# Performance work log

Measured on AMD Instinct MI355X. Metric: run time of the kernel, lower is better.

## Reference

```python
import jax, jax.numpy as jnp
import numpy as np

N = 50000
E = 800000
F_IN = 128
H = 8        # heads
C = 32       # hidden_channels per head
HC = H * C   # 256
NEG_SLOPE = 0.2


def setup_inputs() -> dict:
    key = jax.random.key(0)
    ks = jax.random.split(key, 16)
    s = 0.1
    return {
        'x': jax.random.normal(ks[0], (N, F_IN), jnp.float32),
        'edge_index': jax.random.randint(ks[1], (2, E), 0, N, jnp.int64),
        'edge_weights': jax.random.uniform(ks[2], (E,), jnp.float32),
        'W1': jax.random.normal(ks[3], (F_IN, HC), jnp.float32) * s,
        'att_src1': jax.random.normal(ks[4], (H, C), jnp.float32) * s,
        'att_dst1': jax.random.normal(ks[5], (H, C), jnp.float32) * s,
        'b1': jnp.zeros((HC,), jnp.float32),
        'W2': jax.random.normal(ks[6], (HC, HC), jnp.float32) * s,
        'att_src2': jax.random.normal(ks[7], (H, C), jnp.float32) * s,
        'att_dst2': jax.random.normal(ks[8], (H, C), jnp.float32) * s,
        'b2': jnp.zeros((HC,), jnp.float32),
        'We': jax.random.normal(ks[9], (HC, 1), jnp.float32) * s,
        'be': jnp.zeros((1,), jnp.float32),
        'Wn': jax.random.normal(ks[10], (HC, 1), jnp.float32) * s,
        'bn': jnp.zeros((1,), jnp.float32),
    }


def gat_conv(x, src, dst, W, att_src, att_dst, bias):
    """PyG GATConv (concat=True, eval mode, self-loops already in src/dst)."""
    n = x.shape[0]
    h = (x @ W).reshape(n, H, C)                      # [N,H,C]
    a_s = jnp.sum(h * att_src, axis=-1)               # [N,H]
    a_d = jnp.sum(h * att_dst, axis=-1)               # [N,H]
    e = jax.nn.leaky_relu(a_s[src] + a_d[dst], NEG_SLOPE)  # [E',H]
    m = jax.ops.segment_max(e, dst, num_segments=n)   # segment softmax over dst
    ex = jnp.exp(e - m[dst])
    denom = jax.ops.segment_sum(ex, dst, num_segments=n)
    alpha = ex / (denom[dst] + 1e-16)                 # [E',H]
    out = jax.ops.segment_sum(alpha[..., None] * h[src], dst, num_segments=n)
    return out.reshape(n, HC) + bias


def reference(x, edge_index, edge_weights, W1, att_src1, att_dst1, b1,
              W2, att_src2, att_dst2, b2, We, be, Wn, bn):
    src0, dst0 = edge_index[0], edge_index[1]
    loops = jnp.arange(N, dtype=src0.dtype)
    src = jnp.concatenate([src0, loops])
    dst = jnp.concatenate([dst0, loops])
    # edge_weights is passed to GATConv as edge_attr but unused (edge_dim=None)
    h = jax.nn.relu(gat_conv(x, src, dst, W1, att_src1, att_dst1, b1))
    h = jax.nn.relu(gat_conv(h, src, dst, W2, att_src2, att_dst2, b2))
    edge_pred = (h[src0] * h[dst0]) @ We + be          # [E,1]
    node_pred = h @ Wn + bn                            # [N,1]
    return (edge_pred, node_pred)
```

## Files before the change

kernel.cpp:

```cpp
#include <hip/hip_runtime.h>
#include <hip/hip_bf16.h>

#define NN 50000
#define NE 800000
#define FIN 128
#define HC 256
#define NEG_SLOPE 0.2f

#define GEMM_BLOCKS 782
#define NSB 3321
#define NB_ZERO 196
#define NB_X 6250
#define NB_W1 128
#define NB_W2 256

typedef short bf16x8 __attribute__((ext_vector_type(8)));
typedef float f32x4 __attribute__((ext_vector_type(4)));

__device__ __forceinline__ unsigned short f2bf(float f) {
  unsigned u = __float_as_uint(f);
  u += 0x7fff + ((u >> 16) & 1);
  return (unsigned short)(u >> 16);
}
__device__ __forceinline__ float bf2f(unsigned short s) {
  return __uint_as_float((unsigned)s << 16);
}
__device__ __forceinline__ float bflo(unsigned u) { return __uint_as_float(u << 16); }
__device__ __forceinline__ float bfhi(unsigned u) { return __uint_as_float(u & 0xffff0000u); }

__global__ __launch_bounds__(256) void prep_kernel(
    const float* __restrict__ X, unsigned short* __restrict__ Xh,
    const float* __restrict__ W1, unsigned short* __restrict__ W1th,
    unsigned short* __restrict__ W1tl, const float* __restrict__ W2,
    unsigned short* __restrict__ W2th, unsigned short* __restrict__ W2tl,
    int* __restrict__ counts, int* __restrict__ tmp) {
  int b = blockIdx.x, t = threadIdx.x;
  if (b < NB_ZERO) {
    int i = b * 256 + t;
    if (i < NN) { counts[i] = 0; tmp[i] = 0; }
  } else if (b < NB_ZERO + NB_X) {
    int i = (b - NB_ZERO) * 256 + t;
    float4 v = ((const float4*)X)[i];
    ushort4 h;
    h.x = f2bf(v.x); h.y = f2bf(v.y); h.z = f2bf(v.z); h.w = f2bf(v.w);
    ((ushort4*)Xh)[i] = h;
  } else if (b < NB_ZERO + NB_X + NB_W1) {
    int j = (b - NB_ZERO - NB_X) * 256 + t;
    int n = j >> 7, k = j & 127;
    float v = W1[k * HC + n];
    unsigned short h = f2bf(v);
    W1th[j] = h;
    W1tl[j] = f2bf(v - bf2f(h));
  } else {
    int j = (b - NB_ZERO - NB_X - NB_W1) * 256 + t;
    int n = j >> 8, k = j & 255;
    float v = W2[k * HC + n];
    unsigned short h = f2bf(v);
    W2th[j] = h;
    W2tl[j] = f2bf(v - bf2f(h));
  }
}

__global__ __launch_bounds__(256) void gemm_coef(
    const unsigned short* __restrict__ A, const unsigned short* __restrict__ Bth,
    const unsigned short* __restrict__ Btl, const float* __restrict__ att_s,
    const float* __restrict__ att_d, unsigned short* __restrict__ Cb,
    float* __restrict__ a_s, float* __restrict__ a_d, int M, int K,
    const int* __restrict__ ei, const int* __restrict__ rowptr,
    int* __restrict__ tmpc, int2* __restrict__ ce) {
  __shared__ unsigned short smem[128 * 136];

  int bid = blockIdx.x, t = threadIdx.x;
  if (bid >= GEMM_BLOCKS) {
    int e = (bid - GEMM_BLOCKS) * 256 + t;
    if (e < NE + NN) {
      int s, d, id;
      if (e < NE) { s = ei[e]; d = ei[NE + e]; id = e; }
      else { s = d = e - NE; id = -1; }
      int pos = rowptr[d] + atomicAdd(&tmpc[d], 1);
      ce[pos] = make_int2(s, id);
    }
    return;
  }

  int w = t >> 6, lane = t & 63;
  int quad = lane >> 4, lrow = lane & 15;
  int m0 = (bid >> 1) * 128, n0 = (bid & 1) * 128;
  int wm = (w >> 1) * 64, wn = (w & 1) * 64;

  const unsigned short* arow[4];
#pragma unroll
  for (int mi = 0; mi < 4; ++mi) {
    int gm = m0 + wm + mi * 16 + lrow;
    if (gm >= M) gm = M - 1;
    arow[mi] = A + (size_t)gm * K + quad * 8;
  }

  f32x4 acc[4][4] = {};

  for (int k0 = 0; k0 < K; k0 += 32) {
#pragma unroll
    for (int i = 0; i < 2; ++i) {
      int idx = t + i * 256;
      int row = idx >> 2, q = idx & 3;
      size_t gb = (size_t)(n0 + row) * K + k0 + q * 8;
      *(uint4*)(smem + row * 40 + q * 8) = *(const uint4*)(Bth + gb);
      *(uint4*)(smem + 5120 + row * 40 + q * 8) = *(const uint4*)(Btl + gb);
    }
    __syncthreads();

    bf16x8 fa[4];
#pragma unroll
    for (int mi = 0; mi < 4; ++mi) fa[mi] = *(const bf16x8*)(arow[mi] + k0);
#pragma unroll
    for (int ni = 0; ni < 4; ++ni) {
      bf16x8 fbh = *(const bf16x8*)(smem + (wn + ni * 16 + lrow) * 40 + quad * 8);
      bf16x8 fbl = *(const bf16x8*)(smem + 5120 + (wn + ni * 16 + lrow) * 40 + quad * 8);
#pragma unroll
      for (int mi = 0; mi < 4; ++mi) {
        acc[mi][ni] = __builtin_amdgcn_mfma_f32_16x16x32_bf16(fa[mi], fbh, acc[mi][ni], 0, 0, 0);
        acc[mi][ni] = __builtin_amdgcn_mfma_f32_16x16x32_bf16(fa[mi], fbl, acc[mi][ni], 0, 0, 0);
      }
    }
    __syncthreads();
  }

#pragma unroll
  for (int mi = 0; mi < 4; ++mi) {
#pragma unroll
    for (int r = 0; r < 4; ++r) {
      int row = wm + mi * 16 + quad * 4 + r;
#pragma unroll
      for (int ni = 0; ni < 4; ++ni) {
        int col = wn + ni * 16 + lrow;
        smem[row * 136 + col] = f2bf(acc[mi][ni][r]);
      }
    }
  }
  __syncthreads();

  {
    int row = t >> 1, half = t & 1;
    int gm = m0 + row;
    if (gm < M) {
      float ps0 = 0.f, ps1 = 0.f, pd0 = 0.f, pd1 = 0.f;
#pragma unroll
      for (int j = 0; j < 8; ++j) {
        uint4 v = *(const uint4*)(smem + row * 136 + half * 64 + j * 8);
        int gc = n0 + half * 64 + j * 8;
        *(uint4*)(Cb + (size_t)gm * HC + gc) = v;
        float4 s0 = *(const float4*)(att_s + gc);
        float4 s1 = *(const float4*)(att_s + gc + 4);
        float4 d0 = *(const float4*)(att_d + gc);
        float4 d1 = *(const float4*)(att_d + gc + 4);
        float f0 = bflo(v.x), f1 = bfhi(v.x), f2 = bflo(v.y), f3 = bfhi(v.y);
        float f4 = bflo(v.z), f5 = bfhi(v.z), f6 = bflo(v.w), f7 = bfhi(v.w);
        float ss = f0 * s0.x + f1 * s0.y + f2 * s0.z + f3 * s0.w +
                   f4 * s1.x + f5 * s1.y + f6 * s1.z + f7 * s1.w;
        float dd = f0 * d0.x + f1 * d0.y + f2 * d0.z + f3 * d0.w +
                   f4 * d1.x + f5 * d1.y + f6 * d1.z + f7 * d1.w;
        if (j < 4) { ps0 += ss; pd0 += dd; }
        else       { ps1 += ss; pd1 += dd; }
      }
      int hb2 = (n0 >> 5) + half * 2;
      a_s[gm * 8 + hb2] = ps0;
      a_s[gm * 8 + hb2 + 1] = ps1;
      a_d[gm * 8 + hb2] = pd0;
      a_d[gm * 8 + hb2 + 1] = pd1;
    }
  }
}

__global__ void hist_kernel(const int* __restrict__ ei, int* __restrict__ counts) {
  int e = blockIdx.x * 256 + threadIdx.x;
  if (e < NE) atomicAdd(&counts[ei[NE + e]], 1);
}

__global__ void scan1(const int* __restrict__ counts, int* __restrict__ scanbuf,
                      int* __restrict__ bsum) {
  __shared__ int sd[256];
  int t = threadIdx.x;
  int i = blockIdx.x * 256 + t;
  int v = (i < NN) ? counts[i] + 1 : 0;
  sd[t] = v;
  __syncthreads();
#pragma unroll
  for (int off = 1; off < 256; off <<= 1) {
    int x = (t >= off) ? sd[t - off] : 0;
    __syncthreads();
    sd[t] += x;
    __syncthreads();
  }
  if (i < NN) scanbuf[i] = sd[t];
  if (t == 255) bsum[blockIdx.x] = sd[255];
}

__global__ void scan2(const int* __restrict__ bsum, int* __restrict__ boff, int nb) {
  __shared__ int sd[256];
  int t = threadIdx.x;
  int v = (t < nb) ? bsum[t] : 0;
  sd[t] = v;
  __syncthreads();
#pragma unroll
  for (int off = 1; off < 256; off <<= 1) {
    int x = (t >= off) ? sd[t - off] : 0;
    __syncthreads();
    sd[t] += x;
    __syncthreads();
  }
  if (t < nb) boff[t] = sd[t] - v;
}

__global__ void scan3(const int* __restrict__ scanbuf, const int* __restrict__ boff,
                      int* __restrict__ rowptr) {
  int i = blockIdx.x * 256 + threadIdx.x;
  if (i < NN) rowptr[i + 1] = scanbuf[i] + boff[blockIdx.x];
  if (i == 0) rowptr[0] = 0;
}

__global__ __launch_bounds__(256) void agg_kernel(
    const unsigned short* __restrict__ htb, const float* __restrict__ a_s,
    const float* __restrict__ a_d, const int* __restrict__ rowptr,
    const int2* __restrict__ ce, const float* __restrict__ bias,
    unsigned short* __restrict__ outb,
    const float* __restrict__ Wn, const float* __restrict__ bn,
    float* __restrict__ outn) {
  int d = blockIdx.x * 8 + (threadIdx.x >> 5);
  if (d >= NN) return;
  int l = threadIdx.x & 31;
  int hh = l >> 2;
  float adh = a_d[d * 8 + hh];
  int r0 = rowptr[d], r1 = rowptr[d + 1];
  float denom = 0.f;
  float4 acc0 = {0.f, 0.f, 0.f, 0.f};
  float4 acc1 = {0.f, 0.f, 0.f, 0.f};
  for (int r = r0; r < r1; r += 4) {
    int s[4];
    float as_[4];
    uint4 q[4];
    bool ok[4];
#pragma unroll
    for (int j = 0; j < 4; ++j) {
      int rj = r + j;
      ok[j] = rj < r1;
      rj = ok[j] ? rj : r1 - 1;
      s[j] = ce[rj].x;
    }
#pragma unroll
    for (int j = 0; j < 4; ++j) {
      as_[j] = a_s[s[j] * 8 + hh];
      q[j] = ((const uint4*)(htb + (size_t)s[j] * HC))[l];
    }
#pragma unroll
    for (int j = 0; j < 4; ++j) {
      float e = as_[j] + adh;
      e = e > 0.f ? e : NEG_SLOPE * e;
      float w = ok[j] ? __expf(e) : 0.f;
      denom += w;
      acc0.x += w * bflo(q[j].x);
      acc0.y += w * bfhi(q[j].x);
      acc0.z += w * bflo(q[j].y);
      acc0.w += w * bfhi(q[j].y);
      acc1.x += w * bflo(q[j].z);
      acc1.y += w * bfhi(q[j].z);
      acc1.z += w * bflo(q[j].w);
      acc1.w += w * bfhi(q[j].w);
    }
  }
  float dv = 1.f / denom;
  float4 b0 = *(const float4*)(bias + l * 8);
  float4 b1 = *(const float4*)(bias + l * 8 + 4);
  float4 o0, o1;
  o0.x = fmaxf(fmaf(acc0.x, dv, b0.x), 0.f);
  o0.y = fmaxf(fmaf(acc0.y, dv, b0.y), 0.f);
  o0.z = fmaxf(fmaf(acc0.z, dv, b0.z), 0.f);
  o0.w = fmaxf(fmaf(acc0.w, dv, b0.w), 0.f);
  o1.x = fmaxf(fmaf(acc1.x, dv, b1.x), 0.f);
  o1.y = fmaxf(fmaf(acc1.y, dv, b1.y), 0.f);
  o1.z = fmaxf(fmaf(acc1.z, dv, b1.z), 0.f);
  o1.w = fmaxf(fmaf(acc1.w, dv, b1.w), 0.f);
  uint4 pb;
  pb.x = (unsigned)f2bf(o0.x) | ((unsigned)f2bf(o0.y) << 16);
  pb.y = (unsigned)f2bf(o0.z) | ((unsigned)f2bf(o0.w) << 16);
  pb.z = (unsigned)f2bf(o1.x) | ((unsigned)f2bf(o1.y) << 16);
  pb.w = (unsigned)f2bf(o1.z) | ((unsigned)f2bf(o1.w) << 16);
  ((uint4*)(outb + (size_t)d * HC))[l] = pb;
  if (outn) {
    const float4* wnp = (const float4*)(Wn + l * 8);
    float4 w0 = wnp[0], w1 = wnp[1];
    float p = o0.x * w0.x + o0.y * w0.y + o0.z * w0.z + o0.w * w0.w +
              o1.x * w1.x + o1.y * w1.y + o1.z * w1.z + o1.w * w1.w;
#pragma unroll
    for (int off = 1; off <= 16; off <<= 1) p += __shfl_xor(p, off);
    if (l == 0) outn[d] = p + bn[0];
  }
}

__global__ __launch_bounds__(256) void edge_pred_kernel(
    const unsigned short* __restrict__ h2b, const int* __restrict__ rowptr,
    const int2* __restrict__ ce, const float* __restrict__ We,
    const float* __restrict__ be, float* __restrict__ out) {
  int d = blockIdx.x * 4 + (threadIdx.x >> 6);
  if (d >= NN) return;
  int lane = threadIdx.x & 63;
  int g = lane >> 4, l = lane & 15;
  float b = be[0];

  const uint4* rowd = (const uint4*)(h2b + (size_t)d * HC + l * 16);
  uint4 qd0 = rowd[0], qd1 = rowd[1];
  float wd[16];
  {
    const float4* wep = (const float4*)(We + l * 16);
    float4 w0 = wep[0], w1 = wep[1], w2 = wep[2], w3 = wep[3];
    wd[0] = bflo(qd0.x) * w0.x;  wd[1] = bfhi(qd0.x) * w0.y;
    wd[2] = bflo(qd0.y) * w0.z;  wd[3] = bfhi(qd0.y) * w0.w;
    wd[4] = bflo(qd0.z) * w1.x;  wd[5] = bfhi(qd0.z) * w1.y;
    wd[6] = bflo(qd0.w) * w1.z;  wd[7] = bfhi(qd0.w) * w1.w;
    wd[8] = bflo(qd1.x) * w2.x;  wd[9] = bfhi(qd1.x) * w2.y;
    wd[10] = bflo(qd1.y) * w2.z; wd[11] = bfhi(qd1.y) * w2.w;
    wd[12] = bflo(qd1.z) * w3.x; wd[13] = bfhi(qd1.z) * w3.y;
    wd[14] = bflo(qd1.w) * w3.z; wd[15] = bfhi(qd1.w) * w3.w;
  }

  int r0 = rowptr[d], r1 = rowptr[d + 1];
  for (int r = r0; r < r1; r += 8) {
    int rr0 = r + g, rr1 = r + 4 + g;
    int s0 = 0, id0 = -1, s1 = 0, id1 = -1;
    if (rr0 < r1) { int2 p = ce[rr0]; s0 = p.x; id0 = p.y; }
    if (rr1 < r1) { int2 p = ce[rr1]; s1 = p.x; id1 = p.y; }
    const uint4* ra = (const uint4*)(h2b + (size_t)s0 * HC + l * 16);
    const uint4* rb = (const uint4*)(h2b + (size_t)s1 * HC + l * 16);
    uint4 a0 = ra[0], a1 = ra[1];
    uint4 c0 = rb[0], c1 = rb[1];
    float p0 = bflo(a0.x) * wd[0] + bfhi(a0.x) * wd[1] + bflo(a0.y) * wd[2] +
               bfhi(a0.y) * wd[3] + bflo(a0.z) * wd[4] + bfhi(a0.z) * wd[5] +
               bflo(a0.w) * wd[6] + bfhi(a0.w) * wd[7] + bflo(a1.x) * wd[8] +
               bfhi(a1.x) * wd[9] + bflo(a1.y) * wd[10] + bfhi(a1.y) * wd[11] +
               bflo(a1.z) * wd[12] + bfhi(a1.z) * wd[13] + bflo(a1.w) * wd[14] +
               bfhi(a1.w) * wd[15];
    float p1 = bflo(c0.x) * wd[0] + bfhi(c0.x) * wd[1] + bflo(c0.y) * wd[2] +
               bfhi(c0.y) * wd[3] + bflo(c0.z) * wd[4] + bfhi(c0.z) * wd[5] +
               bflo(c0.w) * wd[6] + bfhi(c0.w) * wd[7] + bflo(c1.x) * wd[8] +
               bfhi(c1.x) * wd[9] + bflo(c1.y) * wd[10] + bfhi(c1.y) * wd[11] +
               bflo(c1.z) * wd[12] + bfhi(c1.z) * wd[13] + bflo(c1.w) * wd[14] +
               bfhi(c1.w) * wd[15];
#pragma unroll
    for (int off = 1; off <= 8; off <<= 1) {
      p0 += __shfl_xor(p0, off);
      p1 += __shfl_xor(p1, off);
    }
    if (l == 0) {
      if (id0 >= 0) out[id0] = p0 + b;
      if (id1 >= 0) out[id1] = p1 + b;
    }
  }
}

extern "C" void kernel_launch(void* const* d_in, const int* in_sizes, int n_in,
                              void* d_out, int out_size, void* d_ws, size_t ws_size,
                              hipStream_t stream) {
  const float* x  = (const float*)d_in[0];
  const int* ei   = (const int*)d_in[1];
  const float* W1 = (const float*)d_in[3];
  const float* as1 = (const float*)d_in[4];
  const float* ad1 = (const float*)d_in[5];
  const float* b1 = (const float*)d_in[6];
  const float* W2 = (const float*)d_in[7];
  const float* as2 = (const float*)d_in[8];
  const float* ad2 = (const float*)d_in[9];
  const float* b2 = (const float*)d_in[10];
  const float* We = (const float*)d_in[11];
  const float* be = (const float*)d_in[12];
  const float* Wn = (const float*)d_in[13];
  const float* bn = (const float*)d_in[14];
  float* out = (float*)d_out;

  char* wsp = (char*)d_ws;
  auto alloc = [&](size_t bytes) {
    char* p = wsp;
    wsp += (bytes + 255) & ~(size_t)255;
    return p;
  };
  unsigned short* hbA = (unsigned short*)alloc((size_t)NN * HC * 2);
  unsigned short* h1b = (unsigned short*)alloc((size_t)NN * HC * 2);
  unsigned short* hbB = (unsigned short*)alloc((size_t)NN * HC * 2);
  float* a_s = (float*)alloc((size_t)NN * 8 * 4);
  float* a_d = (float*)alloc((size_t)NN * 8 * 4);
  int* rowptr = (int*)alloc((size_t)(NN + 1) * 4);
  int2* ce = (int2*)alloc((size_t)(NE + NN + 8) * 8);
  int* counts = (int*)alloc((size_t)NN * 4);
  int* tmp = (int*)alloc((size_t)NN * 4);
  int* scanbuf = (int*)alloc((size_t)NN * 4);
  int* bsum = (int*)alloc(256 * 4);
  int* boff = (int*)alloc(256 * 4);
  unsigned short* W1th = (unsigned short*)alloc((size_t)FIN * HC * 2);
  unsigned short* W1tl = (unsigned short*)alloc((size_t)FIN * HC * 2);
  unsigned short* W2th = (unsigned short*)alloc((size_t)HC * HC * 2);
  unsigned short* W2tl = (unsigned short*)alloc((size_t)HC * HC * 2);

  unsigned short* xh = h1b;

  const int NB = (NN + 255) / 256;

  prep_kernel<<<NB_ZERO + NB_X + NB_W1 + NB_W2, 256, 0, stream>>>(
      x, xh, W1, W1th, W1tl, W2, W2th, W2tl, counts, tmp);
  hist_kernel<<<(NE + 255) / 256, 256, 0, stream>>>(ei, counts);
  scan1<<<NB, 256, 0, stream>>>(counts, scanbuf, bsum);
  scan2<<<1, 256, 0, stream>>>(bsum, boff, NB);
  scan3<<<NB, 256, 0, stream>>>(scanbuf, boff, rowptr);

  gemm_coef<<<GEMM_BLOCKS + NSB, 256, 0, stream>>>(
      xh, W1th, W1tl, as1, ad1, hbA, a_s, a_d, NN, FIN, ei, rowptr, tmp, ce);
  agg_kernel<<<NN / 8, 256, 0, stream>>>(hbA, a_s, a_d, rowptr, ce, b1, h1b,
                                         (const float*)nullptr, (const float*)nullptr,
                                         (float*)nullptr);

  gemm_coef<<<GEMM_BLOCKS, 256, 0, stream>>>(
      h1b, W2th, W2tl, as2, ad2, hbA, a_s, a_d, NN, HC,
      (const int*)nullptr, rowptr, tmp, ce);
  agg_kernel<<<NN / 8, 256, 0, stream>>>(hbA, a_s, a_d, rowptr, ce, b2, hbB,
                                         Wn, bn, out + NE);

  edge_pred_kernel<<<NN / 4, 256, 0, stream>>>(hbB, rowptr, ce, We, be, out);
}
```

Measured before the change: 460.6 us.

## Stage A tile in LDS and compute attention coefficients from accumulators via shuffles

New measurement: 446.3 us. 3.1% less time.

```diff
diff --git a/kernel.cpp b/kernel.cpp
--- a/kernel.cpp
+++ b/kernel.cpp
@@ -68,7 +68,9 @@
     float* __restrict__ a_s, float* __restrict__ a_d, int M, int K,
     const int* __restrict__ ei, const int* __restrict__ rowptr,
     int* __restrict__ tmpc, int2* __restrict__ ce) {
-  __shared__ unsigned short smem[128 * 136];
+  __shared__ unsigned short sA[128 * 40];
+  __shared__ unsigned short sBh[128 * 40];
+  __shared__ unsigned short sBl[128 * 40];
 
   int bid = blockIdx.x, t = threadIdx.x;
   if (bid >= GEMM_BLOCKS) {
@@ -88,14 +90,6 @@
   int m0 = (bid >> 1) * 128, n0 = (bid & 1) * 128;
   int wm = (w >> 1) * 64, wn = (w & 1) * 64;
 
-  const unsigned short* arow[4];
-#pragma unroll
-  for (int mi = 0; mi < 4; ++mi) {
-    int gm = m0 + wm + mi * 16 + lrow;
-    if (gm >= M) gm = M - 1;
-    arow[mi] = A + (size_t)gm * K + quad * 8;
-  }
-
   f32x4 acc[4][4] = {};
 
   for (int k0 = 0; k0 < K; k0 += 32) {
@@ -103,19 +97,24 @@
     for (int i = 0; i < 2; ++i) {
       int idx = t + i * 256;
       int row = idx >> 2, q = idx & 3;
+      int gm = m0 + row;
+      if (gm >= M) gm = M - 1;
+      size_t ga = (size_t)gm * K + k0 + q * 8;
       size_t gb = (size_t)(n0 + row) * K + k0 + q * 8;
-      *(uint4*)(smem + row * 40 + q * 8) = *(const uint4*)(Bth + gb);
-      *(uint4*)(smem + 5120 + row * 40 + q * 8) = *(const uint4*)(Btl + gb);
+      *(uint4*)(sA + row * 40 + q * 8) = *(const uint4*)(A + ga);
+      *(uint4*)(sBh + row * 40 + q * 8) = *(const uint4*)(Bth + gb);
+      *(uint4*)(sBl + row * 40 + q * 8) = *(const uint4*)(Btl + gb);
     }
     __syncthreads();
 
     bf16x8 fa[4];
 #pragma unroll
-    for (int mi = 0; mi < 4; ++mi) fa[mi] = *(const bf16x8*)(arow[mi] + k0);
+    for (int mi = 0; mi < 4; ++mi)
+      fa[mi] = *(const bf16x8*)(sA + (wm + mi * 16 + lrow) * 40 + quad * 8);
 #pragma unroll
     for (int ni = 0; ni < 4; ++ni) {
-      bf16x8 fbh = *(const bf16x8*)(smem + (wn + ni * 16 + lrow) * 40 + quad * 8);
-      bf16x8 fbl = *(const bf16x8*)(smem + 5120 + (wn + ni * 16 + lrow) * 40 + quad * 8);
+      bf16x8 fbh = *(const bf16x8*)(sBh + (wn + ni * 16 + lrow) * 40 + quad * 8);
+      bf16x8 fbl = *(const bf16x8*)(sBl + (wn + ni * 16 + lrow) * 40 + quad * 8);
 #pragma unroll
       for (int mi = 0; mi < 4; ++mi) {
         acc[mi][ni] = __builtin_amdgcn_mfma_f32_16x16x32_bf16(fa[mi], fbh, acc[mi][ni], 0, 0, 0);
@@ -125,48 +124,45 @@
     __syncthreads();
   }
 
+  float vs[4], vd[4];
+#pragma unroll
+  for (int ni = 0; ni < 4; ++ni) {
+    int gn = n0 + wn + ni * 16 + lrow;
+    vs[ni] = att_s[gn];
+    vd[ni] = att_d[gn];
+  }
+  int hb = (n0 + wn) >> 5;
+
 #pragma unroll
   for (int mi = 0; mi < 4; ++mi) {
 #pragma unroll
     for (int r = 0; r < 4; ++r) {
-      int row = wm + mi * 16 + quad * 4 + r;
-#pragma unroll
-      for (int ni = 0; ni < 4; ++ni) {
-        int col = wn + ni * 16 + lrow;
-        smem[row * 136 + col] = f2bf(acc[mi][ni][r]);
+      int gm = m0 + wm + mi * 16 + quad * 4 + r;
+      bool rowok = gm < M;
+      if (rowok) {
+#pragma unroll
+        for (int ni = 0; ni < 4; ++ni) {
+          int gn = n0 + wn + ni * 16 + lrow;
+          Cb[(size_t)gm * HC + gn] = f2bf(acc[mi][ni][r]);
+        }
       }
-    }
-  }
-  __syncthreads();
-
-  {
-    int row = t >> 1, half = t & 1;
-    int gm = m0 + row;
-    if (gm < M) {
-      float ps0 = 0.f, ps1 = 0.f, pd0 = 0.f, pd1 = 0.f;
-#pragma unroll
-      for (int j = 0; j < 8; ++j) {
-        uint4 v = *(const uint4*)(smem + row * 136 + half * 64 + j * 8);
-        int gc = n0 + half * 64 + j * 8;
-        *(uint4*)(Cb + (size_t)gm * HC + gc) = v;
-        float4 s0 = *(const float4*)(att_s + gc);
-        float4 s1 = *(const float4*)(att_s + gc + 4);
-        float4 d0 = *(const float4*)(att_d + gc);
-        float4 d1 = *(const float4*)(att_d + gc + 4);
-        float f0 = bflo(v.x), f1 = bfhi(v.x), f2 = bflo(v.y), f3 = bfhi(v.y);
-        float f4 = bflo(v.z), f5 = bfhi(v.z), f6 = bflo(v.w), f7 = bfhi(v.w);
-        float ss = f0 * s0.x + f1 * s0.y + f2 * s0.z + f3 * s0.w +
-                   f4 * s1.x + f5 * s1.y + f6 * s1.z + f7 * s1.w;
-        float dd = f0 * d0.x + f1 * d0.y + f2 * d0.z + f3 * d0.w +
-                   f4 * d1.x + f5 * d1.y + f6 * d1.z + f7 * d1.w;
-        if (j < 4) { ps0 += ss; pd0 += dd; }
-        else       { ps1 += ss; pd1 += dd; }
+      float pse = acc[mi][0][r] * vs[0] + acc[mi][1][r] * vs[1];
+      float pso = acc[mi][2][r] * vs[2] + acc[mi][3][r] * vs[3];
+      float pde = acc[mi][0][r] * vd[0] + acc[mi][1][r] * vd[1];
+      float pdo = acc[mi][2][r] * vd[2] + acc[mi][3][r] * vd[3];
+#pragma unroll
+      for (int off = 1; off <= 8; off <<= 1) {
+        pse += __shfl_xor(pse, off);
+        pso += __shfl_xor(pso, off);
+        pde += __shfl_xor(pde, off);
+        pdo += __shfl_xor(pdo, off);
       }
-      int hb2 = (n0 >> 5) + half * 2;
-      a_s[gm * 8 + hb2] = ps0;
-      a_s[gm * 8 + hb2 + 1] = ps1;
-      a_d[gm * 8 + hb2] = pd0;
-      a_d[gm * 8 + hb2 + 1] = pd1;
+      if (lrow == 0 && rowok) {
+        a_s[gm * 8 + hb] = pse;
+        a_s[gm * 8 + hb + 1] = pso;
+        a_d[gm * 8 + hb] = pde;
+        a_d[gm * 8 + hb + 1] = pdo;
+      }
     }
   }
 }
```
